# Kernel optimization log

Hardware: AMD Instinct MI355X
Metric: run time of the kernel (lower is better)

Reference implementation:

```python
import jax, jax.numpy as jnp
import numpy as np

HEADS = 16


def setup_inputs() -> dict:
    key = jax.random.key(0)
    ks = jax.random.split(key, 7)
    B, N, MEM, DIM = 2, 2048, 2048, 1024
    J = MEM + N
    x = jax.random.normal(ks[0], (B, N, DIM), dtype=jnp.float32)
    mem = jax.random.normal(ks[1], (B, MEM, DIM), dtype=jnp.float32)
    expire_mask = jax.random.uniform(ks[2], (B, 1, 1, J), dtype=jnp.float32)
    Wq = jax.random.normal(ks[3], (DIM, DIM), dtype=jnp.float32) * 0.02
    Wkv = jax.random.normal(ks[4], (DIM, 2 * DIM), dtype=jnp.float32) * 0.02
    Wo = jax.random.normal(ks[5], (DIM, DIM), dtype=jnp.float32) * 0.02
    bo = jnp.zeros((DIM,), dtype=jnp.float32)
    return {"x": x, "mem": mem, "expire_mask": expire_mask,
            "Wq": Wq, "Wkv": Wkv, "Wo": Wo, "bo": bo}


def reference(x, mem, expire_mask, Wq, Wkv, Wo, bo):
    b, n, dim = x.shape
    h = HEADS
    d = dim // h
    scale = d ** -0.5
    mem_len = mem.shape[1]

    q = x @ Wq                                   # [b, n, dim]
    context = jnp.concatenate([mem, x], axis=1)  # [b, j, dim]
    kv = context @ Wkv                           # [b, j, 2*dim]
    k, v = jnp.split(kv, 2, axis=-1)

    def to_heads(t):
        bb, nn, _ = t.shape
        return t.reshape(bb, nn, h, d).transpose(0, 2, 1, 3)  # b h n d

    q, k, v = map(to_heads, (q, k, v))

    dots = jnp.einsum('bhid,bhjd->bhij', q, k) * scale  # [b,h,n,j]
    j_len = dots.shape[-1]
    # causal mask with memory offset: position i attends to j <= i + mem_len
    i_idx = jnp.arange(n)[:, None]
    j_idx = jnp.arange(j_len)[None, :]
    causal = j_idx > (i_idx + mem_len)           # True => masked
    dots = jnp.where(causal[None, None], -jnp.inf, dots)

    attn = jax.nn.softmax(dots, axis=-1)
    attn = attn * expire_mask                    # post-softmax expire gating

    out = jnp.einsum('bhij,bhjd->bhid', attn, v)  # [b,h,n,d]
    out = out.transpose(0, 2, 1, 3).reshape(b, n, dim)
    return out @ Wo + bo
```

## Files before the change

kernel.cpp:

```cpp
#include <hip/hip_runtime.h>
#include <cstdint>

typedef __bf16 bf16_t;
typedef __attribute__((ext_vector_type(2))) __bf16 bf16x2;
typedef __attribute__((ext_vector_type(4))) __bf16 bf16x4;
typedef __attribute__((ext_vector_type(8))) __bf16 bf16x8;
typedef __attribute__((ext_vector_type(4))) float f32x4;
typedef __attribute__((ext_vector_type(16))) float f32x16;
typedef __attribute__((ext_vector_type(4))) int i32x4;

constexpr int Bx = 2, Nx = 2048, MEMx = 2048, Jx = 4096, DIMx = 1024, Hx = 16, HDx = 64;

__device__ __forceinline__ void gload_lds16(const bf16_t* g, bf16_t* lds) {
  __builtin_amdgcn_global_load_lds(
      (const __attribute__((address_space(1))) unsigned int*)g,
      (__attribute__((address_space(3))) unsigned int*)lds, 16, 0, 0);
}

__device__ __forceinline__ int pk2(float a, float b) {
  bf16x2 t;
  t[0] = (bf16_t)a;
  t[1] = (bf16_t)b;
  return __builtin_bit_cast(int, t);
}

__device__ __forceinline__ void pl32swap(int& a, int& b) {
  asm volatile("v_permlane32_swap_b32 %0, %1" : "+v"(a), "+v"(b));
}

__global__ void k_build_bf16(const float* __restrict__ x, const float* __restrict__ mem,
                             bf16_t* __restrict__ xb, bf16_t* __restrict__ ctxb) {
  const int XT = Bx * Nx * DIMx;
  const int CT = Bx * Jx * DIMx;
  for (int i = blockIdx.x * blockDim.x + threadIdx.x; i < XT + CT;
       i += gridDim.x * blockDim.x) {
    if (i < XT) {
      xb[i] = (bf16_t)x[i];
    } else {
      int c = i - XT;
      int bb = c / (Jx * DIMx);
      int rr = c % (Jx * DIMx);
      int j = rr / DIMx, d = rr % DIMx;
      float v = (j < MEMx) ? mem[(int64_t)(bb * MEMx + j) * DIMx + d]
                           : x[(int64_t)(bb * Nx + (j - MEMx)) * DIMx + d];
      ctxb[c] = (bf16_t)v;
    }
  }
}

__global__ void k_transpose_w(const float* __restrict__ W, bf16_t* __restrict__ WT,
                              int K, int Nc) {
  int total = K * Nc;
  for (int i = blockIdx.x * blockDim.x + threadIdx.x; i < total;
       i += gridDim.x * blockDim.x) {
    int n = i / K, k = i % K;
    WT[i] = (bf16_t)W[(int64_t)k * Nc + n];
  }
}

template <int OUTF32>
__launch_bounds__(256)
__global__ void k_gemm_bt(const bf16_t* __restrict__ A, const bf16_t* __restrict__ BT,
                          void* __restrict__ Cv, const float* __restrict__ bias,
                          const float* __restrict__ gate, int gate_col0, float scale,
                          int M, int Nc, int K) {
  __shared__ bf16_t As[128 * 32];
  __shared__ bf16_t Bs[128 * 32];
  const int tid = threadIdx.x;
  const int w = tid >> 6, l = tid & 63;
  const int lr = l & 15, lg = l >> 4;
  const int m0 = blockIdx.y * 128, n0 = blockIdx.x * 128;
  const int wm = (w >> 1) * 64, wn = (w & 1) * 64;

  const int srow = w * 16 + (l >> 2);
  const int scol = (l & 3) * 8;
  const bf16_t* ga0 = A + (int64_t)(m0 + srow) * K + scol;
  const bf16_t* gb0 = BT + (int64_t)(n0 + srow) * K + scol;
  bf16_t* lA = As + w * 512;
  bf16_t* lB = Bs + w * 512;

  f32x4 acc[4][4] = {};

  for (int k0 = 0; k0 < K; k0 += 32) {
    __syncthreads();
    gload_lds16(ga0 + k0, lA);
    gload_lds16(ga0 + (int64_t)64 * K + k0, lA + 2048);
    gload_lds16(gb0 + k0, lB);
    gload_lds16(gb0 + (int64_t)64 * K + k0, lB + 2048);
    __syncthreads();

    bf16x8 af[4], bfr[4];
#pragma unroll
    for (int t = 0; t < 4; ++t)
      af[t] = *(const bf16x8*)(As + (wm + t * 16 + lr) * 32 + lg * 8);
#pragma unroll
    for (int t = 0; t < 4; ++t)
      bfr[t] = *(const bf16x8*)(Bs + (wn + t * 16 + lr) * 32 + lg * 8);
#pragma unroll
    for (int mt = 0; mt < 4; ++mt)
#pragma unroll
      for (int nt = 0; nt < 4; ++nt)
        acc[mt][nt] = __builtin_amdgcn_mfma_f32_16x16x32_bf16(af[mt], bfr[nt],
                                                              acc[mt][nt], 0, 0, 0);
  }

#pragma unroll
  for (int mt = 0; mt < 4; ++mt) {
#pragma unroll
    for (int nt = 0; nt < 4; ++nt) {
      int col = n0 + wn + nt * 16 + lr;
#pragma unroll
      for (int r = 0; r < 4; ++r) {
        int row = m0 + wm + mt * 16 + lg * 4 + r;
        float v = acc[mt][nt][r] * scale;
        if (gate != nullptr && col >= gate_col0) v *= gate[row];
        if constexpr (OUTF32) {
          ((float*)Cv)[(int64_t)row * Nc + col] = v + bias[col];
        } else {
          ((bf16_t*)Cv)[(int64_t)row * Nc + col] = (bf16_t)v;
        }
      }
    }
  }
}

__launch_bounds__(256)
__global__ void k_attn(const bf16_t* __restrict__ Q, const bf16_t* __restrict__ KV,
                       bf16_t* __restrict__ Hout) {
  __shared__ bf16_t Ks[2][64 * 64];
  __shared__ bf16_t Vs[2][64 * 80];

  const int tid = threadIdx.x;
  const int w = tid >> 6, l = tid & 63;
  const int ql = l & 31, hi = l >> 5;
  const int b = blockIdx.z, h = blockIdx.y;
  const int qi = b ? (gridDim.x - 1 - blockIdx.x) : blockIdx.x;
  const int q0 = qi * 128;

  const bf16_t* Qb = Q + ((int64_t)b * Nx) * DIMx + h * HDx;
  const bf16_t* Kb = KV + ((int64_t)b * Jx) * (2 * DIMx) + h * HDx;
  const bf16_t* Vb = Kb + DIMx;

  const int qrow = q0 + w * 32 + ql;

  bf16x8 qf[4];
#pragma unroll
  for (int dt = 0; dt < 4; ++dt)
    qf[dt] = *(const bf16x8*)(Qb + (int64_t)qrow * DIMx + dt * 16 + hi * 8);

  int koff[2][4], voff[2][4];
#pragma unroll
  for (int jb = 0; jb < 2; ++jb)
#pragma unroll
    for (int dt = 0; dt < 4; ++dt)
      koff[jb][dt] = (jb * 32 + ql) * 128 + (((dt * 2 + hi) * 16) ^ ((ql & 7) * 16));
#pragma unroll
  for (int db = 0; db < 2; ++db)
#pragma unroll
    for (int jt = 0; jt < 4; ++jt)
      voff[db][jt] = (db * 32 + ql) * 160 +
                     (((jt * 2 + hi) * 16) ^ (((db * 4 + (ql >> 3)) & 7) * 16));

  f32x16 o[2] = {};
  float mrun = -1e30f, lsum = 0.f;

  const int ksrow = w * 16 + (l >> 3);
  const int kscol = ((l & 7) ^ (l >> 3)) * 8;
  const int jend = (Jx < q0 + 128 + MEMx) ? Jx : (q0 + 128 + MEMx);
  const int nt_tiles = jend >> 6;
  const f32x16 z16 = {};

  auto stageK = [&](int bufi, int j0) {
    bf16_t* kd = &Ks[bufi][0] + w * 1024;
    const bf16_t* src = Kb + (int64_t)(j0 + ksrow) * 2048 + kscol;
    gload_lds16(src, kd);
    gload_lds16(src + (int64_t)8 * 2048, kd + 512);
  };
  auto stageV = [&](int bufi, int j0) {
#pragma unroll
    for (int t = 0; t < 2; ++t) {
      int vj = t * 32 + w * 8 + (l >> 3);
      int vd0 = (l & 7) * 8;
      bf16x8 vv = *(const bf16x8*)(Vb + (int64_t)(j0 + vj) * 2048 + vd0);
      int chx = ((t * 4 + w) ^ (l & 7)) * 16;
#pragma unroll
      for (int i = 0; i < 8; ++i)
        *(bf16_t*)((char*)&Vs[bufi][0] + (vd0 + i) * 160 + chx + (l >> 3) * 2) = vv[i];
    }
  };

  stageK(0, 0);
  stageV(0, 0);
  __syncthreads();

  for (int t = 0; t < nt_tiles; ++t) {
    const int cur = t & 1;
    const int j0 = t << 6;
    if (t + 1 < nt_tiles) {
      stageK(cur ^ 1, j0 + 64);
      stageV(cur ^ 1, j0 + 64);
    }
    const char* KsC = (const char*)&Ks[cur][0];
    const char* VsC = (const char*)&Vs[cur][0];

    f32x16 s[2];
    __builtin_amdgcn_s_setprio(1);
#pragma unroll
    for (int jb = 0; jb < 2; ++jb) {
      f32x16 acc = z16;
#pragma unroll
      for (int dt = 0; dt < 4; ++dt) {
        bf16x8 kf = *(const bf16x8*)(KsC + koff[jb][dt]);
        acc = __builtin_amdgcn_mfma_f32_32x32x16_bf16(kf, qf[dt], acc, 0, 0, 0);
      }
      s[jb] = acc;
    }
    __builtin_amdgcn_s_setprio(0);

    if (j0 + 63 > q0 + MEMx) {
#pragma unroll
      for (int jb = 0; jb < 2; ++jb)
#pragma unroll
        for (int r = 0; r < 16; ++r) {
          int j = j0 + jb * 32 + (r & 3) + (r >> 2) * 8 + hi * 4;
          if (j > qrow + MEMx) s[jb][r] = -1e30f;
        }
    }

    f32x16 tv = __builtin_elementwise_max(s[0], s[1]);
    float t8[8], t4[4];
#pragma unroll
    for (int i = 0; i < 8; ++i) t8[i] = fmaxf(tv[i], tv[i + 8]);
#pragma unroll
    for (int i = 0; i < 4; ++i) t4[i] = fmaxf(t8[i], t8[i + 4]);
    float tm = fmaxf(fmaxf(t4[0], t4[1]), fmaxf(t4[2], t4[3]));
    tm = fmaxf(tm, __shfl_xor(tm, 32));

    if (!__all(tm <= mrun + 8.f)) {
      float mnew = fmaxf(mrun, tm);
      float al = exp2f(mrun - mnew);
      mrun = mnew;
      lsum *= al;
#pragma unroll
      for (int db = 0; db < 2; ++db)
#pragma unroll
        for (int r = 0; r < 16; ++r) o[db][r] *= al;
    }

#pragma unroll
    for (int jb = 0; jb < 2; ++jb)
#pragma unroll
      for (int r = 0; r < 16; ++r) s[jb][r] = exp2f(s[jb][r] - mrun);

    f32x16 av = s[0] + s[1];
    float a8[8], a4[4];
#pragma unroll
    for (int i = 0; i < 8; ++i) a8[i] = av[i] + av[i + 8];
#pragma unroll
    for (int i = 0; i < 4; ++i) a4[i] = a8[i] + a8[i + 4];
    float ps = (a4[0] + a4[1]) + (a4[2] + a4[3]);
    ps += __shfl_xor(ps, 32);
    lsum += ps;

    bf16x8 pfrag[4];
#pragma unroll
    for (int jb = 0; jb < 2; ++jb) {
      int pw[8];
#pragma unroll
      for (int g = 0; g < 8; ++g) pw[g] = pk2(s[jb][2 * g], s[jb][2 * g + 1]);
      pl32swap(pw[0], pw[2]);
      pl32swap(pw[1], pw[3]);
      pl32swap(pw[4], pw[6]);
      pl32swap(pw[5], pw[7]);
      i32x4 f0 = {pw[0], pw[1], pw[2], pw[3]};
      i32x4 f1 = {pw[4], pw[5], pw[6], pw[7]};
      pfrag[jb * 2] = __builtin_bit_cast(bf16x8, f0);
      pfrag[jb * 2 + 1] = __builtin_bit_cast(bf16x8, f1);
    }

    __builtin_amdgcn_s_setprio(1);
#pragma unroll
    for (int db = 0; db < 2; ++db)
#pragma unroll
      for (int jt = 0; jt < 4; ++jt) {
        bf16x8 vf = *(const bf16x8*)(VsC + voff[db][jt]);
        o[db] = __builtin_amdgcn_mfma_f32_32x32x16_bf16(vf, pfrag[jt], o[db], 0, 0, 0);
      }
    __builtin_amdgcn_s_setprio(0);

    __syncthreads();
  }

  float inv = 1.f / lsum;
#pragma unroll
  for (int db = 0; db < 2; ++db)
#pragma unroll
    for (int g = 0; g < 4; ++g) {
      bf16x4 ov;
#pragma unroll
      for (int r = 0; r < 4; ++r) ov[r] = (bf16_t)(o[db][g * 4 + r] * inv);
      *(bf16x4*)(Hout + (int64_t)(b * Nx + qrow) * DIMx + h * HDx + db * 32 + g * 8 +
                 hi * 4) = ov;
    }
}

extern "C" void kernel_launch(void* const* d_in, const int* in_sizes, int n_in,
                              void* d_out, int out_size, void* d_ws, size_t ws_size,
                              hipStream_t stream) {
  const float* x    = (const float*)d_in[0];
  const float* mem  = (const float*)d_in[1];
  const float* expm = (const float*)d_in[2];
  const float* Wq   = (const float*)d_in[3];
  const float* Wkv  = (const float*)d_in[4];
  const float* Wo   = (const float*)d_in[5];
  const float* bo   = (const float*)d_in[6];
  float* out = (float*)d_out;

  bf16_t* p = (bf16_t*)d_ws;
  bf16_t* xb   = p; p += (size_t)Bx * Nx * DIMx;
  bf16_t* ctxb = p; p += (size_t)Bx * Jx * DIMx;
  bf16_t* WqT  = p; p += (size_t)DIMx * DIMx;
  bf16_t* WkvT = p; p += (size_t)DIMx * 2 * DIMx;
  bf16_t* WoT  = p; p += (size_t)DIMx * DIMx;
  bf16_t* Qb   = p; p += (size_t)Bx * Nx * DIMx;
  bf16_t* KVb  = p; p += (size_t)Bx * Jx * 2 * DIMx;
  bf16_t* Ho   = p; p += (size_t)Bx * Nx * DIMx;

  k_build_bf16<<<4096, 256, 0, stream>>>(x, mem, xb, ctxb);
  k_transpose_w<<<1024, 256, 0, stream>>>(Wq, WqT, DIMx, DIMx);
  k_transpose_w<<<2048, 256, 0, stream>>>(Wkv, WkvT, DIMx, 2 * DIMx);
  k_transpose_w<<<1024, 256, 0, stream>>>(Wo, WoT, DIMx, DIMx);

  const float qscale = 0.125f * 1.4426950408889634f;
  k_gemm_bt<0><<<dim3(1024 / 128, 4096 / 128), 256, 0, stream>>>(
      xb, WqT, Qb, nullptr, nullptr, 0x7fffffff, qscale, Bx * Nx, DIMx, DIMx);
  k_gemm_bt<0><<<dim3(2048 / 128, 8192 / 128), 256, 0, stream>>>(
      ctxb, WkvT, KVb, nullptr, expm, DIMx, 1.0f, Bx * Jx, 2 * DIMx, DIMx);
  k_attn<<<dim3(Nx / 128, Hx, Bx), 256, 0, stream>>>(Qb, KVb, Ho);
  k_gemm_bt<1><<<dim3(1024 / 128, 4096 / 128), 256, 0, stream>>>(
      Ho, WoT, out, bo, nullptr, 0x7fffffff, 1.0f, Bx * Nx, DIMx, DIMx);
}
```

Baseline: 308.6 us.

## Double-buffer GEMM LDS tiles and defer V LDS writes past attention compute

The bf16 GEMM kernel now keeps two LDS buffers per operand and prefetches the next K-slice while running MFMAs on the current one, which removes one barrier per iteration. In the attention kernel, the V tile for the next step is loaded into registers at the start of each iteration and only written (transposed) into LDS after the PV MFMAs, so the global-load latency overlaps with compute. The GEMM's LDS footprint doubles and the attention kernel holds extra registers for V, which may lower occupancy.

```diff
diff --git a/kernel.cpp b/kernel.cpp
--- a/kernel.cpp
+++ b/kernel.cpp
@@ -64,8 +64,8 @@
                           void* __restrict__ Cv, const float* __restrict__ bias,
                           const float* __restrict__ gate, int gate_col0, float scale,
                           int M, int Nc, int K) {
-  __shared__ bf16_t As[128 * 32];
-  __shared__ bf16_t Bs[128 * 32];
+  __shared__ bf16_t As[2][128 * 32];
+  __shared__ bf16_t Bs[2][128 * 32];
   const int tid = threadIdx.x;
   const int w = tid >> 6, l = tid & 63;
   const int lr = l & 15, lg = l >> 4;
@@ -76,32 +76,40 @@
   const int scol = (l & 3) * 8;
   const bf16_t* ga0 = A + (int64_t)(m0 + srow) * K + scol;
   const bf16_t* gb0 = BT + (int64_t)(n0 + srow) * K + scol;
-  bf16_t* lA = As + w * 512;
-  bf16_t* lB = Bs + w * 512;
-
-  f32x4 acc[4][4] = {};
-
-  for (int k0 = 0; k0 < K; k0 += 32) {
-    __syncthreads();
+
+  auto stage = [&](int bufi, int k0) {
+    bf16_t* lA = &As[bufi][0] + w * 512;
+    bf16_t* lB = &Bs[bufi][0] + w * 512;
     gload_lds16(ga0 + k0, lA);
     gload_lds16(ga0 + (int64_t)64 * K + k0, lA + 2048);
     gload_lds16(gb0 + k0, lB);
     gload_lds16(gb0 + (int64_t)64 * K + k0, lB + 2048);
-    __syncthreads();
+  };
+
+  f32x4 acc[4][4] = {};
+
+  stage(0, 0);
+  __syncthreads();
+
+  const int nsteps = K >> 5;
+  for (int t = 0; t < nsteps; ++t) {
+    const int cur = t & 1;
+    if (t + 1 < nsteps) stage(cur ^ 1, (t + 1) << 5);
 
     bf16x8 af[4], bfr[4];
 #pragma unroll
-    for (int t = 0; t < 4; ++t)
-      af[t] = *(const bf16x8*)(As + (wm + t * 16 + lr) * 32 + lg * 8);
-#pragma unroll
-    for (int t = 0; t < 4; ++t)
-      bfr[t] = *(const bf16x8*)(Bs + (wn + t * 16 + lr) * 32 + lg * 8);
+    for (int q = 0; q < 4; ++q)
+      af[q] = *(const bf16x8*)(&As[cur][0] + (wm + q * 16 + lr) * 32 + lg * 8);
+#pragma unroll
+    for (int q = 0; q < 4; ++q)
+      bfr[q] = *(const bf16x8*)(&Bs[cur][0] + (wn + q * 16 + lr) * 32 + lg * 8);
 #pragma unroll
     for (int mt = 0; mt < 4; ++mt)
 #pragma unroll
       for (int nt = 0; nt < 4; ++nt)
         acc[mt][nt] = __builtin_amdgcn_mfma_f32_16x16x32_bf16(af[mt], bfr[nt],
                                                               acc[mt][nt], 0, 0, 0);
+    __syncthreads();
   }
 
 #pragma unroll
@@ -170,35 +178,46 @@
   const int nt_tiles = jend >> 6;
   const f32x16 z16 = {};
 
+  const bf16_t* vsrc0 = Vb + (int64_t)(w * 8 + (l >> 3)) * 2048 + (l & 7) * 8;
+  const int vd0 = (l & 7) * 8;
+  const int vrow2 = (l >> 3) * 2;
+  const int chx0 = ((w) ^ (l & 7)) * 16;
+  const int chx1 = ((4 + w) ^ (l & 7)) * 16;
+
   auto stageK = [&](int bufi, int j0) {
     bf16_t* kd = &Ks[bufi][0] + w * 1024;
     const bf16_t* src = Kb + (int64_t)(j0 + ksrow) * 2048 + kscol;
     gload_lds16(src, kd);
     gload_lds16(src + (int64_t)8 * 2048, kd + 512);
   };
-  auto stageV = [&](int bufi, int j0) {
-#pragma unroll
-    for (int t = 0; t < 2; ++t) {
-      int vj = t * 32 + w * 8 + (l >> 3);
-      int vd0 = (l & 7) * 8;
-      bf16x8 vv = *(const bf16x8*)(Vb + (int64_t)(j0 + vj) * 2048 + vd0);
-      int chx = ((t * 4 + w) ^ (l & 7)) * 16;
-#pragma unroll
-      for (int i = 0; i < 8; ++i)
-        *(bf16_t*)((char*)&Vs[bufi][0] + (vd0 + i) * 160 + chx + (l >> 3) * 2) = vv[i];
-    }
+  auto loadV = [&](int j0, bf16x8& a, bf16x8& c) {
+    const bf16_t* s = vsrc0 + (int64_t)j0 * 2048;
+    a = *(const bf16x8*)s;
+    c = *(const bf16x8*)(s + (int64_t)32 * 2048);
   };
-
+  auto writeV = [&](int bufi, bf16x8 a, bf16x8 c) {
+    char* base = (char*)&Vs[bufi][0];
+#pragma unroll
+    for (int i = 0; i < 8; ++i)
+      *(bf16_t*)(base + (vd0 + i) * 160 + chx0 + vrow2) = a[i];
+#pragma unroll
+    for (int i = 0; i < 8; ++i)
+      *(bf16_t*)(base + (vd0 + i) * 160 + chx1 + vrow2) = c[i];
+  };
+
+  bf16x8 vA, vC;
   stageK(0, 0);
-  stageV(0, 0);
+  loadV(0, vA, vC);
+  writeV(0, vA, vC);
   __syncthreads();
 
   for (int t = 0; t < nt_tiles; ++t) {
     const int cur = t & 1;
     const int j0 = t << 6;
-    if (t + 1 < nt_tiles) {
+    const bool pf = (t + 1 < nt_tiles);
+    if (pf) {
       stageK(cur ^ 1, j0 + 64);
-      stageV(cur ^ 1, j0 + 64);
+      loadV(j0 + 64, vA, vC);
     }
     const char* KsC = (const char*)&Ks[cur][0];
     const char* VsC = (const char*)&Vs[cur][0];
@@ -288,6 +307,7 @@
       }
     __builtin_amdgcn_s_setprio(0);
 
+    if (pf) writeV(cur ^ 1, vA, vC);
     __syncthreads();
   }
 
```

Measured after the change: 302.0 us. 1.02x faster.
